# Kernel optimization log

Measured on AMD Instinct MI355X. Metric: run time of the kernel, lower is better.

## Reference

```python
import jax, jax.numpy as jnp
import numpy as np

STRIDE = 1
PAD = 1

def setup_inputs() -> dict:
    key = jax.random.key(0)
    k1, k2 = jax.random.split(key)
    x = jax.random.normal(k1, (32, 128, 56, 56), dtype=jnp.float32)
    weight = jax.random.normal(k2, (256, 128, 3, 3), dtype=jnp.float32) * 0.1
    b = jnp.zeros((256,), dtype=jnp.float32)
    return {"x": x, "weight": weight, "b": b}

def reference(x, weight, b):
    # Binarize weights with sign (matches torch.sign: sign(0)=0), then plain conv2d.
    bw = jnp.sign(weight)
    out = jax.lax.conv_general_dilated(
        x, bw,
        window_strides=(STRIDE, STRIDE),
        padding=((PAD, PAD), (PAD, PAD)),
        dimension_numbers=("NCHW", "OIHW", "NCHW"),
    )
    return out + b[None, :, None, None]
```

## Files before the change

kernel.cpp:

```cpp
#include <hip/hip_runtime.h>
#include <hip/hip_bf16.h>

typedef __attribute__((ext_vector_type(8))) short bf16x8;
typedef __attribute__((ext_vector_type(4))) float f32x4;

#define CIN   128
#define COUT  256
#define NIMG  32
#define HWDIM 56
#define HPAD  58
#define KTOT  1152
#define HWIMG 3136
#define MTOT  100352
#define BK    64
#define NT    18

__device__ __forceinline__ void gload16(const void* g, void* l) {
  __builtin_amdgcn_global_load_lds((const __attribute__((address_space(1))) void*)g,
                                   (__attribute__((address_space(3))) void*)l,
                                   16, 0, 0);
}

__global__ __launch_bounds__(256)
void prep_all(const float* __restrict__ x, const float* __restrict__ w,
              __hip_bfloat16* __restrict__ xp, __hip_bfloat16* __restrict__ wt) {
  __shared__ float tile[CIN * 57];
  const int bid = blockIdx.x;
  const int t = threadIdx.x;
  if (bid < NIMG * HPAD) {
    const int n = bid / HPAD;
    const int h = bid - n * HPAD;
    __hip_bfloat16* dstrow = xp + ((size_t)n * HPAD + h) * HPAD * CIN;
    int4 z; z.x = 0; z.y = 0; z.z = 0; z.w = 0;
    if (h == 0 || h == HPAD - 1) {
      for (int i = t; i < (HPAD * CIN) / 8; i += 256)
        reinterpret_cast<int4*>(dstrow)[i] = z;
      return;
    }
    const float* src = x + (size_t)n * CIN * HWIMG + (size_t)(h - 1) * HWDIM;
    for (int i = t; i < CIN * HWDIM; i += 256) {
      int c = i / HWDIM;
      int wd = i - c * HWDIM;
      tile[c * 57 + wd] = src[(size_t)c * HWIMG + wd];
    }
    if (t < 32) {
      int side = t >> 4;
      reinterpret_cast<int4*>(dstrow + (side ? (HPAD - 1) : 0) * CIN)[t & 15] = z;
    }
    __syncthreads();
    __hip_bfloat16* dst = dstrow + CIN;
    for (int o = t; o < HWDIM * 64; o += 256) {
      int wd = o >> 6;
      int c = (o & 63) * 2;
      __hip_bfloat162 pr;
      pr.x = __float2bfloat16(tile[c * 57 + wd]);
      pr.y = __float2bfloat16(tile[(c + 1) * 57 + wd]);
      *reinterpret_cast<__hip_bfloat162*>(dst + (size_t)wd * CIN + c) = pr;
    }
  } else {
    int o = (bid - NIMG * HPAD) * 256 + t;
    int cout = o / KTOT;
    int r = o - cout * KTOT;
    int tap = r >> 7;
    int cin = r & 127;
    float v = w[((size_t)cout * CIN + cin) * 9 + tap];
    wt[o] = __float2bfloat16(v > 0.f ? 1.f : (v < 0.f ? -1.f : 0.f));
  }
}

__global__ __launch_bounds__(256, 4)
void bconv(const short* __restrict__ xp, const short* __restrict__ wt,
           const float* __restrict__ bias, float* __restrict__ out) {
  __shared__ short lw[128 * BK];
  __shared__ short lx[128 * BK];

  const int tid  = threadIdx.x;
  const int lane = tid & 63;
  const int wv   = tid >> 6;
  const int wm   = wv >> 1;
  const int wn   = wv & 1;

  const int myid = blockIdx.y * 784 + blockIdx.x;
  const int sid  = (myid & 7) * 196 + (myid >> 3);
  const int s0   = (sid >> 1) * 128;
  const int f0   = (sid & 1) * 128;

  const int srow = tid >> 3;
  const int slot = tid & 7;
  const int swz  = slot ^ (srow & 7);

  int xoff[4];
  int woff[4];
#pragma unroll
  for (int r = 0; r < 4; ++r) {
    int m  = s0 + r * 32 + srow;
    int n  = m / HWIMG;
    int hw = m - n * HWIMG;
    int h  = hw / HWDIM;
    int w  = hw - h * HWDIM;
    xoff[r] = ((n * HPAD + h) * HPAD + w) * CIN + swz * 8;
    woff[r] = (f0 + r * 32 + srow) * KTOT + swz * 8;
  }

  f32x4 acc[4][4] = {};

  short* lwdst = &lw[(wv * 8) * BK];
  short* lxdst = &lx[(wv * 8) * BK];

  for (int ks = 0; ks < NT; ++ks) {
    const int tap = ks >> 1;
    const int kh  = tap / 3;
    const int kw  = tap - kh * 3;
    const int xko = (kh * HPAD + kw) * CIN + (ks & 1) * BK;
    const int wko = ks * BK;

    __syncthreads();
#pragma unroll
    for (int r = 0; r < 4; ++r) {
      gload16(wt + woff[r] + wko, lwdst + r * 32 * BK);
      gload16(xp + xoff[r] + xko, lxdst + r * 32 * BK);
    }
    __syncthreads();

    const int rlo = lane & 15;
#pragma unroll
    for (int ksub = 0; ksub < 2; ++ksub) {
      const int sx = (ksub * 4 + (lane >> 4)) ^ (rlo & 7);
      bf16x8 af[4], bx[4];
#pragma unroll
      for (int f = 0; f < 4; ++f)
        af[f] = *(const bf16x8*)&lw[(wm * 64 + f * 16 + rlo) * BK + sx * 8];
#pragma unroll
      for (int f = 0; f < 4; ++f)
        bx[f] = *(const bf16x8*)&lx[(wn * 64 + f * 16 + rlo) * BK + sx * 8];
#pragma unroll
      for (int fm = 0; fm < 4; ++fm)
#pragma unroll
        for (int fn = 0; fn < 4; ++fn)
          acc[fm][fn] = __builtin_amdgcn_mfma_f32_16x16x32_bf16(
              bx[fn], af[fm], acc[fm][fn], 0, 0, 0);
    }
  }

  const int col = lane & 15;
  const int rg  = lane >> 4;
  int nb[4], hwb[4];
#pragma unroll
  for (int fn = 0; fn < 4; ++fn) {
    int m16 = s0 + wn * 64 + fn * 16;
    int n = m16 / HWIMG;
    nb[fn]  = n;
    hwb[fn] = m16 - n * HWIMG + rg * 4;
  }
#pragma unroll
  for (int fm = 0; fm < 4; ++fm) {
    int cc = f0 + wm * 64 + fm * 16 + col;
    float bv = bias[cc];
#pragma unroll
    for (int fn = 0; fn < 4; ++fn) {
      float4 v;
      v.x = acc[fm][fn][0] + bv;
      v.y = acc[fm][fn][1] + bv;
      v.z = acc[fm][fn][2] + bv;
      v.w = acc[fm][fn][3] + bv;
      *reinterpret_cast<float4*>(out + ((size_t)nb[fn] * COUT + cc) * HWIMG + hwb[fn]) = v;
    }
  }
}

extern "C" void kernel_launch(void* const* d_in, const int* in_sizes, int n_in,
                              void* d_out, int out_size, void* d_ws, size_t ws_size,
                              hipStream_t stream) {
  const float* x = (const float*)d_in[0];
  const float* w = (const float*)d_in[1];
  const float* b = (const float*)d_in[2];
  float* out = (float*)d_out;

  const size_t xp_elems = (size_t)NIMG * HPAD * HPAD * CIN;
  __hip_bfloat16* xp = (__hip_bfloat16*)d_ws;
  __hip_bfloat16* wt = xp + xp_elems;

  prep_all<<<NIMG * HPAD + (COUT * KTOT) / 256, 256, 0, stream>>>(x, w, xp, wt);

  dim3 grid(MTOT / 128, COUT / 128);
  bconv<<<grid, 256, 0, stream>>>((const short*)xp, (const short*)wt, b, out);
}
```

Measured before the change: 89.15 us.

## Pre-swizzle weights into MFMA fragment layout and double-buffer activation tiles

The prep kernel now writes sign-binarized weights in a layout that matches the MFMA A-fragment order. The conv kernel can then load weight fragments straight from global memory into registers and drop the LDS weight tile. The activation tile is double-buffered in LDS, with the next stage's global-to-LDS loads issued before the current MFMAs and a partial vmcnt wait replacing the full syncthreads pair. The aim is to hide load latency and halve LDS traffic. The cost is more registers for prefetched fragments, so occupancy is lowered to 3 waves per SIMD.

```diff
diff --git a/kernel.cpp b/kernel.cpp
--- a/kernel.cpp
+++ b/kernel.cpp
@@ -14,6 +14,7 @@
 #define MTOT  100352
 #define BK    64
 #define NT    18
+#define NS    36
 
 __device__ __forceinline__ void gload16(const void* g, void* l) {
   __builtin_amdgcn_global_load_lds((const __attribute__((address_space(1))) void*)g,
@@ -23,7 +24,7 @@
 
 __global__ __launch_bounds__(256)
 void prep_all(const float* __restrict__ x, const float* __restrict__ w,
-              __hip_bfloat16* __restrict__ xp, __hip_bfloat16* __restrict__ wt) {
+              __hip_bfloat16* __restrict__ xp, __hip_bfloat16* __restrict__ wtf) {
   __shared__ float tile[CIN * 57];
   const int bid = blockIdx.x;
   const int t = threadIdx.x;
@@ -60,19 +61,19 @@
   } else {
     int o = (bid - NIMG * HPAD) * 256 + t;
     int cout = o / KTOT;
-    int r = o - cout * KTOT;
-    int tap = r >> 7;
-    int cin = r & 127;
+    int k = o - cout * KTOT;
+    int tap = k >> 7;
+    int cin = k & 127;
     float v = w[((size_t)cout * CIN + cin) * 9 + tap];
-    wt[o] = __float2bfloat16(v > 0.f ? 1.f : (v < 0.f ? -1.f : 0.f));
+    int dst = (((cout >> 4) * NS + (k >> 5)) * 64 + (cout & 15) + (((k >> 3) & 3) << 4)) * 8 + (k & 7);
+    wtf[dst] = __float2bfloat16(v > 0.f ? 1.f : (v < 0.f ? -1.f : 0.f));
   }
 }
 
-__global__ __launch_bounds__(256, 4)
-void bconv(const short* __restrict__ xp, const short* __restrict__ wt,
+__global__ __launch_bounds__(256, 3)
+void bconv(const short* __restrict__ xp, const short* __restrict__ wtf,
            const float* __restrict__ bias, float* __restrict__ out) {
-  __shared__ short lw[128 * BK];
-  __shared__ short lx[128 * BK];
+  __shared__ short lx[2][128 * BK];
 
   const int tid  = threadIdx.x;
   const int lane = tid & 63;
@@ -90,7 +91,6 @@
   const int swz  = slot ^ (srow & 7);
 
   int xoff[4];
-  int woff[4];
 #pragma unroll
   for (int r = 0; r < 4; ++r) {
     int m  = s0 + r * 32 + srow;
@@ -99,47 +99,54 @@
     int h  = hw / HWDIM;
     int w  = hw - h * HWDIM;
     xoff[r] = ((n * HPAD + h) * HPAD + w) * CIN + swz * 8;
-    woff[r] = (f0 + r * 32 + srow) * KTOT + swz * 8;
   }
 
+  const short* wbase = wtf + (size_t)((f0 >> 4) + wm * 4) * NS * 512 + lane * 8;
+
   f32x4 acc[4][4] = {};
+  bf16x8 af[4][2], bx[4][2];
 
-  short* lwdst = &lw[(wv * 8) * BK];
-  short* lxdst = &lx[(wv * 8) * BK];
+#define AF_LOAD(T) \
+  _Pragma("unroll") for (int f = 0; f < 4; ++f) \
+  _Pragma("unroll") for (int ksub = 0; ksub < 2; ++ksub) \
+    af[f][ksub] = *(const bf16x8*)(wbase + ((size_t)f * NS + (T) * 2 + ksub) * 512);
 
-  for (int ks = 0; ks < NT; ++ks) {
-    const int tap = ks >> 1;
-    const int kh  = tap / 3;
-    const int kw  = tap - kh * 3;
-    const int xko = (kh * HPAD + kw) * CIN + (ks & 1) * BK;
-    const int wko = ks * BK;
+#define XKO(T) ((((T) >> 1) / 3 * HPAD + ((T) >> 1) % 3) * CIN + ((T) & 1) * BK)
 
-    __syncthreads();
+#define STAGE_B(C, T) \
+  _Pragma("unroll") for (int r = 0; r < 4; ++r) \
+    gload16(xp + xoff[r] + XKO(T), &lx[C][(r * 32 + wv * 8) * BK]);
+
+  STAGE_B(0, 0)
+  AF_LOAD(0)
+
+  const int rlo = lane & 15;
+  const int kq  = lane >> 4;
+  const int swr = rlo & 7;
+
+  for (int t = 0; t < NT; ++t) {
+    const int cur = t & 1;
+    asm volatile("s_waitcnt vmcnt(8)" ::: "memory");
+    __builtin_amdgcn_s_barrier();
+
+    if (t + 1 < NT) { STAGE_B(cur ^ 1, t + 1) }
+
 #pragma unroll
-    for (int r = 0; r < 4; ++r) {
-      gload16(wt + woff[r] + wko, lwdst + r * 32 * BK);
-      gload16(xp + xoff[r] + xko, lxdst + r * 32 * BK);
-    }
-    __syncthreads();
+    for (int f = 0; f < 4; ++f)
+#pragma unroll
+      for (int ksub = 0; ksub < 2; ++ksub)
+        bx[f][ksub] = *(const bf16x8*)&lx[cur][(wn * 64 + f * 16 + rlo) * BK + ((ksub * 4 + kq) ^ swr) * 8];
 
-    const int rlo = lane & 15;
 #pragma unroll
-    for (int ksub = 0; ksub < 2; ++ksub) {
-      const int sx = (ksub * 4 + (lane >> 4)) ^ (rlo & 7);
-      bf16x8 af[4], bx[4];
-#pragma unroll
-      for (int f = 0; f < 4; ++f)
-        af[f] = *(const bf16x8*)&lw[(wm * 64 + f * 16 + rlo) * BK + sx * 8];
-#pragma unroll
-      for (int f = 0; f < 4; ++f)
-        bx[f] = *(const bf16x8*)&lx[(wn * 64 + f * 16 + rlo) * BK + sx * 8];
+    for (int kk = 0; kk < 2; ++kk)
 #pragma unroll
       for (int fm = 0; fm < 4; ++fm)
 #pragma unroll
         for (int fn = 0; fn < 4; ++fn)
           acc[fm][fn] = __builtin_amdgcn_mfma_f32_16x16x32_bf16(
-              bx[fn], af[fm], acc[fm][fn], 0, 0, 0);
-    }
+              bx[fn][kk], af[fm][kk], acc[fm][fn], 0, 0, 0);
+
+    if (t + 1 < NT) { AF_LOAD(t + 1) }
   }
 
   const int col = lane & 15;
@@ -166,6 +173,9 @@
       *reinterpret_cast<float4*>(out + ((size_t)nb[fn] * COUT + cc) * HWIMG + hwb[fn]) = v;
     }
   }
+#undef AF_LOAD
+#undef XKO
+#undef STAGE_B
 }
 
 extern "C" void kernel_launch(void* const* d_in, const int* in_sizes, int n_in,
@@ -177,11 +187,11 @@
   float* out = (float*)d_out;
 
   const size_t xp_elems = (size_t)NIMG * HPAD * HPAD * CIN;
-  __hip_bfloat16* xp = (__hip_bfloat16*)d_ws;
-  __hip_bfloat16* wt = xp + xp_elems;
+  __hip_bfloat16* xp  = (__hip_bfloat16*)d_ws;
+  __hip_bfloat16* wtf = xp + xp_elems;
 
-  prep_all<<<NIMG * HPAD + (COUT * KTOT) / 256, 256, 0, stream>>>(x, w, xp, wt);
+  prep_all<<<NIMG * HPAD + (COUT * KTOT) / 256, 256, 0, stream>>>(x, w, xp, wtf);
 
   dim3 grid(MTOT / 128, COUT / 128);
-  bconv<<<grid, 256, 0, stream>>>((const short*)xp, (const short*)wt, b, out);
+  bconv<<<grid, 256, 0, stream>>>((const short*)xp, (const short*)wtf, b, out);
 }
```

Measured after the change: 93.53 us. 1.05x slower.

## Double-buffer LDS tiles to overlap global loads with MFMA compute

Applied to the files above, without the earlier changes.

Adds a second LDS buffer for the weight and input tiles so the next K-step is prefetched with direct-to-LDS global loads while the current tile feeds the MFMAs. Each iteration then needs one barrier instead of two. LDS per block doubles to 64KB and the launch-bounds occupancy hint drops from 4 to 2 blocks per CU, so fewer waves are available to hide latency.

```diff
diff --git a/kernel.cpp b/kernel.cpp
--- a/kernel.cpp
+++ b/kernel.cpp
@@ -68,11 +68,11 @@
   }
 }
 
-__global__ __launch_bounds__(256, 4)
+__global__ __launch_bounds__(256, 2)
 void bconv(const short* __restrict__ xp, const short* __restrict__ wt,
            const float* __restrict__ bias, float* __restrict__ out) {
-  __shared__ short lw[128 * BK];
-  __shared__ short lx[128 * BK];
+  __shared__ short lw[2][128 * BK];
+  __shared__ short lx[2][128 * BK];
 
   const int tid  = threadIdx.x;
   const int lane = tid & 63;
@@ -104,35 +104,35 @@
 
   f32x4 acc[4][4] = {};
 
-  short* lwdst = &lw[(wv * 8) * BK];
-  short* lxdst = &lx[(wv * 8) * BK];
+#define XKO(T) ((((T) >> 1) / 3 * HPAD + ((T) >> 1) % 3) * CIN + ((T) & 1) * BK)
+#define STAGE(C, T) \
+  _Pragma("unroll") for (int r = 0; r < 4; ++r) { \
+    gload16(wt + woff[r] + (T) * BK, &lw[C][(r * 32 + wv * 8) * BK]); \
+    gload16(xp + xoff[r] + XKO(T), &lx[C][(r * 32 + wv * 8) * BK]); \
+  }
 
-  for (int ks = 0; ks < NT; ++ks) {
-    const int tap = ks >> 1;
-    const int kh  = tap / 3;
-    const int kw  = tap - kh * 3;
-    const int xko = (kh * HPAD + kw) * CIN + (ks & 1) * BK;
-    const int wko = ks * BK;
+  STAGE(0, 0)
+  asm volatile("s_waitcnt vmcnt(0)" ::: "memory");
+  __builtin_amdgcn_s_barrier();
 
-    __syncthreads();
-#pragma unroll
-    for (int r = 0; r < 4; ++r) {
-      gload16(wt + woff[r] + wko, lwdst + r * 32 * BK);
-      gload16(xp + xoff[r] + xko, lxdst + r * 32 * BK);
-    }
-    __syncthreads();
+  const int rlo = lane & 15;
+  const int kq  = lane >> 4;
+  const int swr = rlo & 7;
 
-    const int rlo = lane & 15;
+  for (int t = 0; t < NT; ++t) {
+    const int cur = t & 1;
+    if (t + 1 < NT) { STAGE(cur ^ 1, t + 1) }
+
 #pragma unroll
     for (int ksub = 0; ksub < 2; ++ksub) {
-      const int sx = (ksub * 4 + (lane >> 4)) ^ (rlo & 7);
+      const int sx = (ksub * 4 + kq) ^ swr;
       bf16x8 af[4], bx[4];
 #pragma unroll
       for (int f = 0; f < 4; ++f)
-        af[f] = *(const bf16x8*)&lw[(wm * 64 + f * 16 + rlo) * BK + sx * 8];
+        af[f] = *(const bf16x8*)&lw[cur][(wm * 64 + f * 16 + rlo) * BK + sx * 8];
 #pragma unroll
       for (int f = 0; f < 4; ++f)
-        bx[f] = *(const bf16x8*)&lx[(wn * 64 + f * 16 + rlo) * BK + sx * 8];
+        bx[f] = *(const bf16x8*)&lx[cur][(wn * 64 + f * 16 + rlo) * BK + sx * 8];
 #pragma unroll
       for (int fm = 0; fm < 4; ++fm)
 #pragma unroll
@@ -140,6 +140,9 @@
           acc[fm][fn] = __builtin_amdgcn_mfma_f32_16x16x32_bf16(
               bx[fn], af[fm], acc[fm][fn], 0, 0, 0);
     }
+
+    asm volatile("s_waitcnt vmcnt(0)" ::: "memory");
+    __builtin_amdgcn_s_barrier();
   }
 
   const int col = lane & 15;
@@ -166,6 +169,8 @@
       *reinterpret_cast<float4*>(out + ((size_t)nb[fn] * COUT + cc) * HWIMG + hwb[fn]) = v;
     }
   }
+#undef XKO
+#undef STAGE
 }
 
 extern "C" void kernel_launch(void* const* d_in, const int* in_sizes, int n_in,
```

Result: slower. 111.9 us (+25.5%).
